# Kernel optimization log

Hardware: AMD Instinct MI355X
Metric: run time of the kernel (lower is better)

The kernel has to match this reference:

```python
import jax, jax.numpy as jnp
import numpy as np

BLOCK_SIZE = 256
N_EMBD = 768
HEAD_SIZE = 768  # == n_embd so RoPE table (dim=n_embd) matches channel pairing


def _rope_tables(T, dim, theta0=10000.0):
    # compute_freq(dim=n_embd, seq_len=block_size, theta_0=10000):
    # theta_j = theta0^(-2j/dim), angle[t, j] = t * theta_j
    j = jnp.arange(dim // 2, dtype=jnp.float32)
    theta = jnp.float32(theta0) ** (-2.0 * j / jnp.float32(dim))
    ang = jnp.arange(T, dtype=jnp.float32)[:, None] * theta[None, :]  # [T, dim/2]
    return jnp.cos(ang), jnp.sin(ang)


def _apply_rope(t, cos, sin):
    # t: [B, T, D]; pair adjacent channels (2j, 2j+1) as complex, rotate.
    B, T, D = t.shape
    tr = t.reshape(B, T, D // 2, 2)
    re, im = tr[..., 0], tr[..., 1]
    out_re = re * cos[None] - im * sin[None]
    out_im = re * sin[None] + im * cos[None]
    return jnp.stack([out_re, out_im], axis=-1).reshape(B, T, D)


def setup_inputs() -> dict:
    key = jax.random.key(0)
    k1, k2, k3, k4 = jax.random.split(key, 4)
    B, T = 128, BLOCK_SIZE
    x = jax.random.normal(k1, (B, T, N_EMBD), dtype=jnp.float32)
    Wq = jax.random.normal(k2, (N_EMBD, HEAD_SIZE), dtype=jnp.float32) * 0.02
    Wk = jax.random.normal(k3, (N_EMBD, HEAD_SIZE), dtype=jnp.float32) * 0.02
    Wv = jax.random.normal(k4, (N_EMBD, HEAD_SIZE), dtype=jnp.float32) * 0.02
    return {"x": x, "Wq": Wq, "Wk": Wk, "Wv": Wv}


def reference(x, Wq, Wk, Wv):
    B, T, C = x.shape
    q = x @ Wq  # [B, T, D]
    k = x @ Wk
    v = x @ Wv
    cos, sin = _rope_tables(T, HEAD_SIZE)
    q = _apply_rope(q, cos, sin)
    k = _apply_rope(k, cos, sin)
    scale = jnp.float32(HEAD_SIZE) ** -0.5
    wei = jnp.einsum('bqd,bkd->bqk', q, k) * scale  # [B, T, T]
    causal = jnp.tril(jnp.ones((T, T), dtype=bool))
    wei = jnp.where(causal[None], wei, -jnp.inf)
    wei = jax.nn.softmax(wei, axis=-1)
    # dropout(p=0.2) is identity in eval/deterministic baseline
    out = jnp.einsum('bqk,bkd->bqd', wei, v)  # [B, T, D]
    return out
```

## Files before the change

kernel.cpp:

```cpp
#include <hip/hip_runtime.h>
#include <hip/hip_bf16.h>
#include <stdint.h>


typedef __attribute__((ext_vector_type(8))) short short8;
typedef __attribute__((ext_vector_type(4))) short short4v;
typedef __attribute__((ext_vector_type(4))) float f32x4;

__device__ __forceinline__ short f2bf(float f) {
    uint32_t u = __float_as_uint(f);
    u += 0x7fffu + ((u >> 16) & 1u);
    return (short)(u >> 16);
}

__global__ __launch_bounds__(256) void cvt_x(const float* __restrict__ x,
                                             short* __restrict__ xb) {
    long i = ((long)blockIdx.x * 256 + threadIdx.x) * 4;
    f32x4 v = *(const f32x4*)(x + i);
    short4v o;
    o.x = f2bf(v.x); o.y = f2bf(v.y); o.z = f2bf(v.z); o.w = f2bf(v.w);
    *(short4v*)(xb + i) = o;
}

__global__ __launch_bounds__(256) void cvt_wt(const float* __restrict__ W,
                                              short* __restrict__ Wt) {
    __shared__ float tile[32][33];
    int d0 = blockIdx.x * 32, c0 = blockIdx.y * 32;
    int tr = threadIdx.x >> 5, tc = threadIdx.x & 31;
    #pragma unroll
    for (int i = 0; i < 32; i += 8)
        tile[tr + i][tc] = W[(long)(c0 + tr + i) * 768 + d0 + tc];
    __syncthreads();
    #pragma unroll
    for (int i = 0; i < 32; i += 8)
        Wt[(long)(d0 + tr + i) * 768 + c0 + tc] = f2bf(tile[tc][tr + i]);
}

__global__ __launch_bounds__(256) void rope_tab(float2* __restrict__ rt) {
    int i = blockIdx.x * 256 + threadIdx.x;
    int t = i / 384, j = i - t * 384;
    const float CE = -0.034603417655f;
    float th = exp2f((float)j * CE);
    float s, c;
    sincosf((float)t * th, &s, &c);
    rt[i] = make_float2(c, s);
}

template <int EPI, int CAUSAL, int SWZ>
__global__ __launch_bounds__(256)
void gemm_bt(const short* __restrict__ A, const short* __restrict__ B,
             void* __restrict__ C, void* __restrict__ C2, void* __restrict__ C3,
             const float2* __restrict__ rt,
             int M, int N, int K, long sA, long sB, long sC, float scale) {
    int bx, by, bz;
    if (SWZ == 1) {
        int p = blockIdx.x + 18 * blockIdx.y;
        int c = p & 7, j = p >> 3;
        int st = j / 18;
        by = c * 32 + st; bx = j - st * 18; bz = 0;
    } else if (SWZ == 2) {
        int p = blockIdx.x + 2 * (blockIdx.y + 2 * blockIdx.z);
        int c = p & 7, j = p >> 3;
        bz = c * 16 + (j >> 2);
        by = (j >> 1) & 1; bx = j & 1;
    } else if (SWZ == 3) {
        int p = blockIdx.x + 6 * (blockIdx.y + 2 * blockIdx.z);
        int c = p & 7, j = p >> 3;
        int bt = j / 12;
        bz = c * 16 + bt;
        int t = j - bt * 12;
        by = t / 6; bx = t - (t / 6) * 6;
    } else {
        bx = blockIdx.x; by = blockIdx.y; bz = blockIdx.z;
    }
    const int m0 = by * 128;
    const int n0 = bx * 128;
    if (CAUSAL == 1 && n0 > m0) return;

    __shared__ short lA[128 * 64];
    __shared__ short lB[128 * 64];
    const short* Ab = A + (long)bz * sA;
    const short* Bb = B + (long)bz * sB;
    const int tid = threadIdx.x;
    const int w = tid >> 6, lane = tid & 63;
    const int wm = (w >> 1) * 64;
    const int wn = (w & 1) * 64;
    const int lrow8 = lane >> 3;
    const int lcol = (((lane & 7) - lrow8) & 7) * 8;
    const int fr = lane & 15;
    const int kq = lane >> 4;

    const int Kend = (CAUSAL == 2) ? (m0 + 128 < K ? m0 + 128 : K) : K;

    f32x4 acc[4][4] = {};

    for (int k0 = 0; k0 < Kend; k0 += 64) {
        #pragma unroll
        for (int i = 0; i < 4; ++i) {
            int seg = i * 4 + w;
            int row = seg * 8 + lrow8;
            const short* ga = Ab + (long)(m0 + row) * K + k0 + lcol;
            __builtin_amdgcn_global_load_lds(
                (const __attribute__((address_space(1))) void*)ga,
                (__attribute__((address_space(3))) void*)(lA + seg * 512),
                16, 0, 0);
            const short* gb = Bb + (long)(n0 + row) * K + k0 + lcol;
            __builtin_amdgcn_global_load_lds(
                (const __attribute__((address_space(1))) void*)gb,
                (__attribute__((address_space(3))) void*)(lB + seg * 512),
                16, 0, 0);
        }
        __syncthreads();

        #pragma unroll
        for (int c = 0; c < 2; ++c) {
            const int sphys = ((c * 4 + kq + fr) & 7) * 8;
            short8 af[4], bfr[4];
            #pragma unroll
            for (int tmi = 0; tmi < 4; ++tmi)
                af[tmi] = *(const short8*)(lA + (wm + fr + tmi * 16) * 64 + sphys);
            #pragma unroll
            for (int tni = 0; tni < 4; ++tni)
                bfr[tni] = *(const short8*)(lB + (wn + fr + tni * 16) * 64 + sphys);
            #pragma unroll
            for (int tmi = 0; tmi < 4; ++tmi)
                #pragma unroll
                for (int tni = 0; tni < 4; ++tni)
                    acc[tmi][tni] = __builtin_amdgcn_mfma_f32_16x16x32_bf16(
                        af[tmi], bfr[tni], acc[tmi][tni], 0, 0, 0);
        }
        __syncthreads();
    }

    const int r0 = wm + (lane >> 4) * 4;
    const int c0 = wn + (lane & 15);

    if (EPI == 2) {
        #pragma unroll
        for (int tmi = 0; tmi < 4; ++tmi)
            #pragma unroll
            for (int tni = 0; tni < 4; ++tni)
                #pragma unroll
                for (int r = 0; r < 4; ++r) {
                    int row = m0 + r0 + tmi * 16 + r;
                    int col = n0 + c0 + tni * 16;
                    ((float*)C)[(long)bz * sC + (long)row * N + col] =
                        acc[tmi][tni][r] * scale;
                }
    } else {
        const int type = (n0 >= 1536) ? 2 : (n0 >= 768 ? 1 : 0);
        const int nl0 = n0 - type * 768;
        if (type < 2) {
            short* dst = (type == 0) ? (short*)C : (short*)C2;
            const int par = lane & 1;
            #pragma unroll
            for (int tmi = 0; tmi < 4; ++tmi)
                #pragma unroll
                for (int tni = 0; tni < 4; ++tni) {
                    int col = nl0 + c0 + tni * 16;
                    const float2* rtc = rt + (col >> 1);
                    #pragma unroll
                    for (int r = 0; r < 4; ++r) {
                        int row = m0 + r0 + tmi * 16 + r;
                        float val = acc[tmi][tni][r];
                        float pv = __shfl_xor(val, 1);
                        float2 cs = rtc[(row & 255) * 384];
                        float re = par ? pv : val;
                        float im = par ? val : pv;
                        float o = par ? (re * cs.y + im * cs.x)
                                      : (re * cs.x - im * cs.y);
                        dst[(long)row * 768 + col] = f2bf(o);
                    }
                }
        } else {
            short* vt = (short*)C3;
            #pragma unroll
            for (int tmi = 0; tmi < 4; ++tmi)
                #pragma unroll
                for (int tni = 0; tni < 4; ++tni) {
                    int col = nl0 + c0 + tni * 16;
                    #pragma unroll
                    for (int r = 0; r < 4; ++r) {
                        int row = m0 + r0 + tmi * 16 + r;
                        vt[((long)(row >> 8) * 768 + col) * 256 + (row & 255)] =
                            f2bf(acc[tmi][tni][r]);
                    }
                }
        }
    }
}

__global__ __launch_bounds__(256) void softmax_p(const float* __restrict__ S,
                                                 short* __restrict__ P) {
    int wv = threadIdx.x >> 6, lane = threadIdx.x & 63;
    int row = blockIdx.x * 4 + wv;
    int t = row & 255;
    f32x4 v = *(const f32x4*)(S + (long)row * 256 + lane * 4);
    float vals[4];
    float m = -1e30f;
    #pragma unroll
    for (int j = 0; j < 4; ++j) {
        int n = lane * 4 + j;
        vals[j] = (n <= t) ? v[j] : -1e30f;
        m = fmaxf(m, vals[j]);
    }
    #pragma unroll
    for (int o = 32; o; o >>= 1) m = fmaxf(m, __shfl_xor(m, o));
    float e[4], sum = 0.f;
    #pragma unroll
    for (int j = 0; j < 4; ++j) { e[j] = __expf(vals[j] - m); sum += e[j]; }
    #pragma unroll
    for (int o = 32; o; o >>= 1) sum += __shfl_xor(sum, o);
    float inv = 1.0f / sum;
    short4v o4;
    o4.x = f2bf(e[0] * inv); o4.y = f2bf(e[1] * inv);
    o4.z = f2bf(e[2] * inv); o4.w = f2bf(e[3] * inv);
    *(short4v*)(P + (long)row * 256 + lane * 4) = o4;
}

extern "C" void kernel_launch(void* const* d_in, const int* in_sizes, int n_in,
                              void* d_out, int out_size, void* d_ws, size_t ws_size,
                              hipStream_t stream) {
    const float* x  = (const float*)d_in[0];
    const float* Wq = (const float*)d_in[1];
    const float* Wk = (const float*)d_in[2];
    const float* Wv = (const float*)d_in[3];

    char* ws = (char*)d_ws;
    short*  xb = (short*)(ws);
    short*  wt = (short*)(ws + 50331648);
    short*  qb = (short*)(ws + 53870592);
    short*  kb = (short*)(ws + 104202240);
    short*  vt = (short*)(ws + 154533888);
    float*  S  = (float*)(ws + 204865536);
    short*  P  = (short*)(ws + 238419968);
    float2* rt = (float2*)(ws + 255197184);

    cvt_x<<<24576, 256, 0, stream>>>(x, xb);
    dim3 gw(24, 24);
    cvt_wt<<<gw, 256, 0, stream>>>(Wq, wt);
    cvt_wt<<<gw, 256, 0, stream>>>(Wk, wt + 589824);
    cvt_wt<<<gw, 256, 0, stream>>>(Wv, wt + 1179648);
    rope_tab<<<384, 256, 0, stream>>>(rt);

    dim3 g1(18, 256, 1);
    gemm_bt<3, 0, 1><<<g1, 256, 0, stream>>>(xb, wt, qb, kb, vt, rt,
                                             32768, 2304, 768, 0, 0, 0, 1.0f);

    dim3 g2(2, 2, 128);
    gemm_bt<2, 1, 2><<<g2, 256, 0, stream>>>(qb, kb, S, nullptr, nullptr, nullptr,
                                             256, 256, 768, 196608, 196608, 65536,
                                             0.0360843918f);

    softmax_p<<<8192, 256, 0, stream>>>(S, P);

    dim3 g3(6, 2, 128);
    gemm_bt<2, 2, 3><<<g3, 256, 0, stream>>>(P, vt, (float*)d_out, nullptr,
                                             nullptr, nullptr, 256, 768, 256,
                                             65536, 196608, 196608, 1.0f);
}
```

Measured before the change: 441.2 us.

## Replace QKV projection GEMM with 256x256-tile double-buffered 8-wave kernel

Adds a dedicated QKV projection kernel using 256x256 output tiles, 512 threads, and double-buffered LDS. Global-to-LDS staging is interleaved at half-tile granularity with MFMA phases under explicit barriers, waitcnt and setprio. The goal is to raise data reuse per block and hide load latency, which matters because this GEMM is the dominant part of the pipeline. The cost is 128KB of LDS per block, which limits occupancy, plus many barriers and heavy register pressure from 32 accumulators. The old generic path for this GEMM is removed.

```diff
diff --git a/kernel.cpp b/kernel.cpp
--- a/kernel.cpp
+++ b/kernel.cpp
@@ -46,6 +46,174 @@
     rt[i] = make_float2(c, s);
 }
 
+__global__ __launch_bounds__(512, 2)
+void qkv256(const short* __restrict__ A, const short* __restrict__ B,
+            short* __restrict__ Q, short* __restrict__ Kb,
+            short* __restrict__ Vt, const float2* __restrict__ rt) {
+    int p = blockIdx.x;
+    int c = p & 7, j = p >> 3;
+    int st = j / 9;
+    int bx = j - st * 9;
+    int by = c * 16 + st;
+    const int m0 = by * 256, n0 = bx * 256;
+
+    __shared__ short lA[2][256 * 64];
+    __shared__ short lB[2][256 * 64];
+
+    const int tid = threadIdx.x;
+    const int w = tid >> 6, lane = tid & 63;
+    const int wm = (w >> 2) * 128;
+    const int wn = (w & 3) * 64;
+    const int lr8 = lane >> 3;
+    const int scol = (((lane & 7) - lr8) & 7) * 8;
+    const int fr = lane & 15, kq = lane >> 4;
+
+    f32x4 acc[8][4] = {};
+    short8 af[4][2];
+    short8 bq[4][2];
+
+#define STAGE_HALF(lX, gX, r0g, h, t) do {                                     \
+    int _buf = (t) & 1;                                                        \
+    _Pragma("unroll")                                                          \
+    for (int _i = 0; _i < 2; ++_i) {                                           \
+        int _rl = (h) * 128 + (w * 2 + _i) * 8;                                \
+        const short* _g = (gX) + (long)((r0g) + _rl + lr8) * 768               \
+                               + (t) * 64 + scol;                              \
+        __builtin_amdgcn_global_load_lds(                                      \
+            (const __attribute__((address_space(1))) void*)_g,                 \
+            (__attribute__((address_space(3))) void*)(&lX[_buf][_rl * 64]),    \
+            16, 0, 0);                                                         \
+    }                                                                          \
+} while (0)
+
+#define LOAD_A(mh, buf) do {                                                   \
+    _Pragma("unroll")                                                          \
+    for (int _t = 0; _t < 4; ++_t)                                             \
+        _Pragma("unroll")                                                      \
+        for (int _k = 0; _k < 2; ++_k)                                         \
+            af[_t][_k] = *(const short8*)(&lA[buf][                            \
+                (wm + (mh) * 64 + _t * 16 + fr) * 64 +                         \
+                ((_k * 4 + kq + fr) & 7) * 8]);                                \
+} while (0)
+
+#define LOAD_B(nh, buf) do {                                                   \
+    _Pragma("unroll")                                                          \
+    for (int _t = 0; _t < 2; ++_t)                                             \
+        _Pragma("unroll")                                                      \
+        for (int _k = 0; _k < 2; ++_k)                                         \
+            bq[(nh) * 2 + _t][_k] = *(const short8*)(&lB[buf][                 \
+                (wn + (nh) * 32 + _t * 16 + fr) * 64 +                         \
+                ((_k * 4 + kq + fr) & 7) * 8]);                                \
+} while (0)
+
+#define MMA_Q(mh, nh) do {                                                     \
+    __builtin_amdgcn_s_setprio(1);                                             \
+    _Pragma("unroll")                                                          \
+    for (int _t = 0; _t < 4; ++_t)                                             \
+        _Pragma("unroll")                                                      \
+        for (int _n = 0; _n < 2; ++_n)                                         \
+            _Pragma("unroll")                                                  \
+            for (int _k = 0; _k < 2; ++_k)                                     \
+                acc[(mh) * 4 + _t][(nh) * 2 + _n] =                            \
+                    __builtin_amdgcn_mfma_f32_16x16x32_bf16(                   \
+                        af[_t][_k], bq[(nh) * 2 + _n][_k],                     \
+                        acc[(mh) * 4 + _t][(nh) * 2 + _n], 0, 0, 0);           \
+    __builtin_amdgcn_s_setprio(0);                                             \
+} while (0)
+
+#define BAR() __builtin_amdgcn_s_barrier()
+#define LGKM0() asm volatile("s_waitcnt lgkmcnt(0)" ::: "memory")
+#define VMC4() asm volatile("s_waitcnt vmcnt(4)" ::: "memory")
+#define VMC0() asm volatile("s_waitcnt vmcnt(0)" ::: "memory")
+
+    STAGE_HALF(lB, B, n0, 0, 0);
+    STAGE_HALF(lB, B, n0, 1, 0);
+    STAGE_HALF(lA, A, m0, 0, 0);
+    STAGE_HALF(lA, A, m0, 1, 0);
+    STAGE_HALF(lB, B, n0, 0, 1);
+    STAGE_HALF(lB, B, n0, 1, 1);
+    VMC4();
+    BAR();
+
+    #pragma unroll 1
+    for (int i = 0; i < 6; ++i) {
+        const int t0 = 2 * i;
+        const bool more = (i < 5);
+        LOAD_A(0, 0); LOAD_B(0, 0);
+        STAGE_HALF(lA, A, m0, 0, t0 + 1);
+        BAR(); LGKM0(); MMA_Q(0, 0); BAR();
+        LOAD_B(1, 0);
+        STAGE_HALF(lA, A, m0, 1, t0 + 1);
+        BAR(); LGKM0(); MMA_Q(0, 1); BAR();
+        LOAD_A(1, 0);
+        if (more) STAGE_HALF(lB, B, n0, 0, t0 + 2);
+        BAR(); LGKM0(); MMA_Q(1, 1); BAR();
+        if (more) { STAGE_HALF(lB, B, n0, 1, t0 + 2); VMC4(); }
+        else      { VMC0(); }
+        BAR(); LGKM0(); MMA_Q(1, 0); BAR();
+        LOAD_A(0, 1); LOAD_B(0, 1);
+        if (more) STAGE_HALF(lA, A, m0, 0, t0 + 2);
+        BAR(); LGKM0(); MMA_Q(0, 0); BAR();
+        LOAD_B(1, 1);
+        if (more) STAGE_HALF(lA, A, m0, 1, t0 + 2);
+        BAR(); LGKM0(); MMA_Q(0, 1); BAR();
+        LOAD_A(1, 1);
+        if (more) STAGE_HALF(lB, B, n0, 0, t0 + 3);
+        BAR(); LGKM0(); MMA_Q(1, 1); BAR();
+        if (more) { STAGE_HALF(lB, B, n0, 1, t0 + 3); VMC4(); }
+        BAR(); LGKM0(); MMA_Q(1, 0); BAR();
+    }
+
+    const int type = (bx >= 6) ? 2 : (bx >= 3 ? 1 : 0);
+    const int nl0 = n0 - type * 768;
+    const int r0 = wm + (lane >> 4) * 4;
+    const int c0 = wn + (lane & 15);
+    if (type < 2) {
+        short* dst = (type == 0) ? Q : Kb;
+        const int par = lane & 1;
+        #pragma unroll
+        for (int tmi = 0; tmi < 8; ++tmi)
+            #pragma unroll
+            for (int tni = 0; tni < 4; ++tni) {
+                int col = nl0 + c0 + tni * 16;
+                const float2* rtc = rt + (col >> 1);
+                #pragma unroll
+                for (int r = 0; r < 4; ++r) {
+                    int row = m0 + r0 + tmi * 16 + r;
+                    float val = acc[tmi][tni][r];
+                    float pv = __shfl_xor(val, 1);
+                    float2 cs = rtc[(row & 255) * 384];
+                    float re = par ? pv : val;
+                    float im = par ? val : pv;
+                    float o = par ? (re * cs.y + im * cs.x)
+                                  : (re * cs.x - im * cs.y);
+                    dst[(long)row * 768 + col] = f2bf(o);
+                }
+            }
+    } else {
+        #pragma unroll
+        for (int tmi = 0; tmi < 8; ++tmi)
+            #pragma unroll
+            for (int tni = 0; tni < 4; ++tni) {
+                int col = nl0 + c0 + tni * 16;
+                #pragma unroll
+                for (int r = 0; r < 4; ++r) {
+                    int row = m0 + r0 + tmi * 16 + r;
+                    Vt[((long)(row >> 8) * 768 + col) * 256 + (row & 255)] =
+                        f2bf(acc[tmi][tni][r]);
+                }
+            }
+    }
+#undef STAGE_HALF
+#undef LOAD_A
+#undef LOAD_B
+#undef MMA_Q
+#undef BAR
+#undef LGKM0
+#undef VMC4
+#undef VMC0
+}
+
 template <int EPI, int CAUSAL, int SWZ>
 __global__ __launch_bounds__(256)
 void gemm_bt(const short* __restrict__ A, const short* __restrict__ B,
@@ -53,12 +221,7 @@
              const float2* __restrict__ rt,
              int M, int N, int K, long sA, long sB, long sC, float scale) {
     int bx, by, bz;
-    if (SWZ == 1) {
-        int p = blockIdx.x + 18 * blockIdx.y;
-        int c = p & 7, j = p >> 3;
-        int st = j / 18;
-        by = c * 32 + st; bx = j - st * 18; bz = 0;
-    } else if (SWZ == 2) {
+    if (SWZ == 2) {
         int p = blockIdx.x + 2 * (blockIdx.y + 2 * blockIdx.z);
         int c = p & 7, j = p >> 3;
         bz = c * 16 + (j >> 2);
@@ -115,10 +278,10 @@
         #pragma unroll
         for (int c = 0; c < 2; ++c) {
             const int sphys = ((c * 4 + kq + fr) & 7) * 8;
-            short8 af[4], bfr[4];
+            short8 afr[4], bfr[4];
             #pragma unroll
             for (int tmi = 0; tmi < 4; ++tmi)
-                af[tmi] = *(const short8*)(lA + (wm + fr + tmi * 16) * 64 + sphys);
+                afr[tmi] = *(const short8*)(lA + (wm + fr + tmi * 16) * 64 + sphys);
             #pragma unroll
             for (int tni = 0; tni < 4; ++tni)
                 bfr[tni] = *(const short8*)(lB + (wn + fr + tni * 16) * 64 + sphys);
@@ -127,7 +290,7 @@
                 #pragma unroll
                 for (int tni = 0; tni < 4; ++tni)
                     acc[tmi][tni] = __builtin_amdgcn_mfma_f32_16x16x32_bf16(
-                        af[tmi], bfr[tni], acc[tmi][tni], 0, 0, 0);
+                        afr[tmi], bfr[tni], acc[tmi][tni], 0, 0, 0);
         }
         __syncthreads();
     }
@@ -147,46 +310,6 @@
                     ((float*)C)[(long)bz * sC + (long)row * N + col] =
                         acc[tmi][tni][r] * scale;
                 }
-    } else {
-        const int type = (n0 >= 1536) ? 2 : (n0 >= 768 ? 1 : 0);
-        const int nl0 = n0 - type * 768;
-        if (type < 2) {
-            short* dst = (type == 0) ? (short*)C : (short*)C2;
-            const int par = lane & 1;
-            #pragma unroll
-            for (int tmi = 0; tmi < 4; ++tmi)
-                #pragma unroll
-                for (int tni = 0; tni < 4; ++tni) {
-                    int col = nl0 + c0 + tni * 16;
-                    const float2* rtc = rt + (col >> 1);
-                    #pragma unroll
-                    for (int r = 0; r < 4; ++r) {
-                        int row = m0 + r0 + tmi * 16 + r;
-                        float val = acc[tmi][tni][r];
-                        float pv = __shfl_xor(val, 1);
-                        float2 cs = rtc[(row & 255) * 384];
-                        float re = par ? pv : val;
-                        float im = par ? val : pv;
-                        float o = par ? (re * cs.y + im * cs.x)
-                                      : (re * cs.x - im * cs.y);
-                        dst[(long)row * 768 + col] = f2bf(o);
-                    }
-                }
-        } else {
-            short* vt = (short*)C3;
-            #pragma unroll
-            for (int tmi = 0; tmi < 4; ++tmi)
-                #pragma unroll
-                for (int tni = 0; tni < 4; ++tni) {
-                    int col = nl0 + c0 + tni * 16;
-                    #pragma unroll
-                    for (int r = 0; r < 4; ++r) {
-                        int row = m0 + r0 + tmi * 16 + r;
-                        vt[((long)(row >> 8) * 768 + col) * 256 + (row & 255)] =
-                            f2bf(acc[tmi][tni][r]);
-                    }
-                }
-        }
     }
 }
 
@@ -243,9 +366,7 @@
     cvt_wt<<<gw, 256, 0, stream>>>(Wv, wt + 1179648);
     rope_tab<<<384, 256, 0, stream>>>(rt);
 
-    dim3 g1(18, 256, 1);
-    gemm_bt<3, 0, 1><<<g1, 256, 0, stream>>>(xb, wt, qb, kb, vt, rt,
-                                             32768, 2304, 768, 0, 0, 0, 1.0f);
+    qkv256<<<1152, 512, 0, stream>>>(xb, wt, qb, kb, vt, rt);
 
     dim3 g2(2, 2, 128);
     gemm_bt<2, 1, 2><<<g2, 256, 0, stream>>>(qb, kb, S, nullptr, nullptr, nullptr,
```

New measurement: 412.5 us. 6.5% less time.
